# Kernel tuning notes

Hardware: AMD Instinct MI355X
Metric: run time of the kernel (lower is better)

Reference implementation:

```python
import jax, jax.numpy as jnp
import numpy as np

N = 50000      # nodes
E = 800000     # edges (avg degree 16)
IN_DIM = 128
H = 4          # attention heads
D = 32         # hidden dim per head
NEG_SLOPE = 0.2


def setup_inputs() -> dict:
    key = jax.random.key(0)
    ks = jax.random.split(key, 9)
    x = jax.random.normal(ks[0], (N, IN_DIM), dtype=jnp.float32)
    src = jax.random.randint(ks[1], (E,), 0, N, dtype=jnp.int64)
    dst = jax.random.randint(ks[2], (E,), 0, N, dtype=jnp.int64)
    # layer 0: IN_DIM -> H*D ; layer 1: H*D -> H*D
    s0 = 1.0 / np.sqrt(IN_DIM)
    s1 = 1.0 / np.sqrt(H * D)
    W1 = jax.random.normal(ks[3], (H * D, IN_DIM), dtype=jnp.float32) * s0
    al1 = jax.random.normal(ks[4], (1, H, D), dtype=jnp.float32) * s1
    ar1 = jax.random.normal(ks[5], (1, H, D), dtype=jnp.float32) * s1
    W2 = jax.random.normal(ks[6], (H * D, H * D), dtype=jnp.float32) * s1
    al2 = jax.random.normal(ks[7], (1, H, D), dtype=jnp.float32) * s1
    ar2 = jax.random.normal(ks[8], (1, H, D), dtype=jnp.float32) * s1
    return {"x": x, "src": src, "dst": dst, "W1": W1, "al1": al1, "ar1": ar1,
            "W2": W2, "al2": al2, "ar2": ar2}


def gat_conv(h, src, dst, W, al, ar):
    """DGL-style GATConv. h: [N, F_in] -> [N, H, D], with ELU activation."""
    feat = (h @ W.T).reshape(N, H, D)                 # [N,H,D]
    el = jnp.sum(feat * al, axis=-1)                  # [N,H] a_l . Wh
    er = jnp.sum(feat * ar, axis=-1)                  # [N,H] a_r . Wh
    e = jax.nn.leaky_relu(el[src] + er[dst], NEG_SLOPE)  # [E,H]
    # numerically stable edge softmax over incoming edges of each dst node
    m = jax.ops.segment_max(e, dst, num_segments=N)   # [N,H]
    ee = jnp.exp(e - m[dst])                          # [E,H]
    denom = jax.ops.segment_sum(ee, dst, num_segments=N)  # [N,H]
    alpha = ee / denom[dst]                           # [E,H]
    msg = feat[src] * alpha[..., None]                # [E,H,D]
    out = jax.ops.segment_sum(msg, dst, num_segments=N)   # [N,H,D]
    return jax.nn.elu(out)


def reference(x, src, dst, W1, al1, ar1, W2, al2, ar2):
    h = gat_conv(x, src, dst, W1, al1, ar1).reshape(N, H * D)  # flatten(1)
    h = gat_conv(h, src, dst, W2, al2, ar2)                    # [N,H,D]
    return jnp.mean(h, axis=1)                                 # [N,D]
```

## Files before the change

### kernel.cpp

```cpp
#include <hip/hip_runtime.h>
#include <cmath>
#include <type_traits>

#define HEADS 4
#define FDIM 128
#define NEG 0.2f
#define NBUCK 8

typedef __attribute__((ext_vector_type(8))) __bf16 bf16x8;
typedef __attribute__((ext_vector_type(8))) _Float16 h16x8;
typedef __attribute__((ext_vector_type(4))) float f32x4;

__global__ __launch_bounds__(256) void prep_kernel(
    const float* __restrict__ W1, const float* __restrict__ al1,
    const float* __restrict__ ar1,
    const float* __restrict__ W2, const float* __restrict__ al2,
    const float* __restrict__ ar2,
    __bf16* __restrict__ wf1, __bf16* __restrict__ wext1,
    __bf16* __restrict__ wf2, __bf16* __restrict__ wext2,
    int* __restrict__ counts, int nb)
{
    const int b = blockIdx.x, tid = threadIdx.x;
    if (b < 256) {
        const float* W = (b < 128) ? W1 : W2;
        __bf16* wf = (b < 128) ? wf1 : wf2;
        int idx = (b & 127) * 256 + tid;
        int j = idx & 7;
        int r = idx >> 3;
        int c = r & 15; r >>= 4;
        int t = r & 7;  r >>= 3;
        int kq = r & 15;
        int hl = r >> 4;
        float v = W[(t * 16 + c) * 128 + kq * 8 + j];
        __bf16 hi = (__bf16)v;
        wf[idx] = (hl == 0) ? hi : (__bf16)(v - (float)hi);
    } else if (b < 258) {
        const float* W  = (b == 256) ? W1 : W2;
        const float* al = (b == 256) ? al1 : al2;
        const float* ar = (b == 256) ? ar1 : ar2;
        __bf16* wext = (b == 256) ? wext1 : wext2;
        __shared__ float val[1024];
        #pragma unroll
        for (int ch = 0; ch < 4; ++ch) {
            int idx = ch * 256 + tid;
            int c = idx >> 7, k = idx & 127;
            int h = c & 3;
            const float* a = (c < 4) ? al : ar;
            float s = 0.f;
            for (int d = 0; d < 32; ++d)
                s += a[h * 32 + d] * W[(h * 32 + d) * 128 + k];
            val[c * 128 + k] = s;
        }
        __syncthreads();
        #pragma unroll
        for (int ch = 0; ch < 16; ++ch) {
            int idx = tid * 16 + ch;
            int j = idx & 7;
            int r = idx >> 3;
            int c = r & 15; r >>= 4;
            int kq = r & 15;
            int hl = r >> 4;
            float v = (c < 8) ? val[c * 128 + kq * 8 + j] : 0.f;
            __bf16 hi = (__bf16)v;
            wext[idx] = (hl == 0) ? hi : (__bf16)(v - (float)hi);
        }
    } else {
        int i0 = ((b - 258) * 256 + tid) * 4;
        if (i0 + 3 < nb) {
            *(int4*)&counts[i0] = make_int4(0, 0, 0, 0);
        } else {
            for (int i = i0; i < nb; ++i) counts[i] = 0;
        }
    }
}

template <typename XT>
__device__ __forceinline__ void gemm_body(
    const XT* __restrict__ X, const bf16x8* __restrict__ wf,
    const bf16x8* __restrict__ wext, _Float16* __restrict__ featH,
    float* __restrict__ el, float* __restrict__ er,
    int nnodes, int tile0, int tend, int stride, bf16x8* lw)
{
    const int tid = threadIdx.x;
    const int wave = tid >> 6, lane = tid & 63;
    const int l15 = lane & 15, quad = lane >> 4;

    int tile = tile0;
    float xr[32], xn[32];

    auto loadX = [&](int tl, float* dst) {
        int nodeA = tl * 64 + wave * 16 + l15;
        bool v = nodeA < nnodes;
        if constexpr (std::is_same<XT, float>::value) {
            const float4* xp = (const float4*)(X + (size_t)nodeA * 128);
            #pragma unroll
            for (int ks = 0; ks < 4; ++ks) {
                float4 a = v ? xp[ks * 8 + quad * 2]     : make_float4(0.f, 0.f, 0.f, 0.f);
                float4 b = v ? xp[ks * 8 + quad * 2 + 1] : make_float4(0.f, 0.f, 0.f, 0.f);
                dst[ks * 8 + 0] = a.x; dst[ks * 8 + 1] = a.y;
                dst[ks * 8 + 2] = a.z; dst[ks * 8 + 3] = a.w;
                dst[ks * 8 + 4] = b.x; dst[ks * 8 + 5] = b.y;
                dst[ks * 8 + 6] = b.z; dst[ks * 8 + 7] = b.w;
            }
        } else {
            const h16x8* xp = (const h16x8*)(X + (size_t)nodeA * 128);
            #pragma unroll
            for (int ks = 0; ks < 4; ++ks) {
                h16x8 hv;
                if (v) {
                    hv = xp[ks * 4 + quad];
                } else {
                    #pragma unroll
                    for (int j = 0; j < 8; ++j) hv[j] = (_Float16)0.f;
                }
                #pragma unroll
                for (int j = 0; j < 8; ++j) dst[ks * 8 + j] = (float)hv[j];
            }
        }
    };

    loadX(tile, xr);
    for (int i = tid; i < 2048; i += 256) lw[i] = wf[i];
    __syncthreads();

    while (true) {
        int next = tile + stride;
        if (next < tend) loadX(next, xn);

        f32x4 acc[9];
        #pragma unroll
        for (int t = 0; t < 9; ++t) acc[t] = (f32x4){0.f, 0.f, 0.f, 0.f};

        #pragma unroll
        for (int ks = 0; ks < 4; ++ks) {
            bf16x8 ahi, alo;
            #pragma unroll
            for (int j = 0; j < 8; ++j) {
                float xv = xr[ks * 8 + j];
                __bf16 h = (__bf16)xv;
                ahi[j] = h;
                alo[j] = (__bf16)(xv - (float)h);
            }
            const int kq = ks * 4 + quad;

            {
                bf16x8 bh = wext[(kq) * 16 + l15];
                bf16x8 bl = wext[(16 + kq) * 16 + l15];
                acc[8] = __builtin_amdgcn_mfma_f32_16x16x32_bf16(ahi, bh, acc[8], 0, 0, 0);
                acc[8] = __builtin_amdgcn_mfma_f32_16x16x32_bf16(alo, bh, acc[8], 0, 0, 0);
                acc[8] = __builtin_amdgcn_mfma_f32_16x16x32_bf16(ahi, bl, acc[8], 0, 0, 0);
            }
            #pragma unroll
            for (int t = 0; t < 8; ++t) {
                bf16x8 bh = lw[(kq * 8 + t) * 16 + l15];
                bf16x8 bl = wf[2048 + (kq * 8 + t) * 16 + l15];
                acc[t] = __builtin_amdgcn_mfma_f32_16x16x32_bf16(ahi, bh, acc[t], 0, 0, 0);
                acc[t] = __builtin_amdgcn_mfma_f32_16x16x32_bf16(alo, bh, acc[t], 0, 0, 0);
                acc[t] = __builtin_amdgcn_mfma_f32_16x16x32_bf16(ahi, bl, acc[t], 0, 0, 0);
            }
        }

        const int nodeC = tile * 64 + wave * 16 + quad * 4;
        #pragma unroll
        for (int r = 0; r < 4; ++r) {
            int gn = nodeC + r;
            if (gn < nnodes) {
                #pragma unroll
                for (int t = 0; t < 8; ++t)
                    featH[(size_t)gn * 128 + t * 16 + l15] = (_Float16)acc[t][r];
            }
        }
        if (l15 < 8) {
            #pragma unroll
            for (int r = 0; r < 4; ++r) {
                int gn = nodeC + r;
                if (gn < nnodes) {
                    if (l15 < 4) el[gn * HEADS + l15] = acc[8][r];
                    else         er[gn * HEADS + (l15 - 4)] = acc[8][r];
                }
            }
        }

        if (next >= tend) break;
        #pragma unroll
        for (int i = 0; i < 32; ++i) xr[i] = xn[i];
        tile = next;
    }
}

__device__ __forceinline__ void hist_body(
    const int* __restrict__ src, const int* __restrict__ dst,
    int* __restrict__ counts, int* __restrict__ rank, int nedges, int shift, int b)
{
    int i0 = (b * 256 + threadIdx.x) * 8;
    if (i0 + 7 < nedges) {
        int4 d0 = *(const int4*)&dst[i0];
        int4 d1 = *(const int4*)&dst[i0 + 4];
        int4 s0 = *(const int4*)&src[i0];
        int4 s1 = *(const int4*)&src[i0 + 4];
        int4 r0, r1;
        r0.x = atomicAdd(&counts[d0.x * NBUCK + (s0.x >> shift)], 1);
        r0.y = atomicAdd(&counts[d0.y * NBUCK + (s0.y >> shift)], 1);
        r0.z = atomicAdd(&counts[d0.z * NBUCK + (s0.z >> shift)], 1);
        r0.w = atomicAdd(&counts[d0.w * NBUCK + (s0.w >> shift)], 1);
        r1.x = atomicAdd(&counts[d1.x * NBUCK + (s1.x >> shift)], 1);
        r1.y = atomicAdd(&counts[d1.y * NBUCK + (s1.y >> shift)], 1);
        r1.z = atomicAdd(&counts[d1.z * NBUCK + (s1.z >> shift)], 1);
        r1.w = atomicAdd(&counts[d1.w * NBUCK + (s1.w >> shift)], 1);
        *(int4*)&rank[i0]     = r0;
        *(int4*)&rank[i0 + 4] = r1;
    } else {
        for (int i = i0; i < nedges; ++i)
            rank[i] = atomicAdd(&counts[dst[i] * NBUCK + (src[i] >> shift)], 1);
    }
}

__device__ __forceinline__ void scatter_body(
    const int* __restrict__ src, const int* __restrict__ dst,
    const int* __restrict__ rank, const int* __restrict__ offsets,
    int* __restrict__ csr_src, int nedges, int shift, int b)
{
    int i0 = (b * 256 + threadIdx.x) * 8;
    if (i0 + 7 < nedges) {
        int4 d0 = *(const int4*)&dst[i0];
        int4 d1 = *(const int4*)&dst[i0 + 4];
        int4 r0 = *(const int4*)&rank[i0];
        int4 r1 = *(const int4*)&rank[i0 + 4];
        int4 s0 = *(const int4*)&src[i0];
        int4 s1 = *(const int4*)&src[i0 + 4];
        csr_src[offsets[d0.x * NBUCK + (s0.x >> shift)] + r0.x] = s0.x;
        csr_src[offsets[d0.y * NBUCK + (s0.y >> shift)] + r0.y] = s0.y;
        csr_src[offsets[d0.z * NBUCK + (s0.z >> shift)] + r0.z] = s0.z;
        csr_src[offsets[d0.w * NBUCK + (s0.w >> shift)] + r0.w] = s0.w;
        csr_src[offsets[d1.x * NBUCK + (s1.x >> shift)] + r1.x] = s1.x;
        csr_src[offsets[d1.y * NBUCK + (s1.y >> shift)] + r1.y] = s1.y;
        csr_src[offsets[d1.z * NBUCK + (s1.z >> shift)] + r1.z] = s1.z;
        csr_src[offsets[d1.w * NBUCK + (s1.w >> shift)] + r1.w] = s1.w;
    } else {
        for (int i = i0; i < nedges; ++i)
            csr_src[offsets[dst[i] * NBUCK + (src[i] >> shift)] + rank[i]] = src[i];
    }
}

__global__ __launch_bounds__(256) void fused_gemm_hist(
    const float* __restrict__ X, const bf16x8* __restrict__ wf,
    const bf16x8* __restrict__ wext, _Float16* __restrict__ featH,
    float* __restrict__ el, float* __restrict__ er, int nnodes,
    int t0, int tend, int gemm_blocks,
    const int* __restrict__ src, const int* __restrict__ dst,
    int* __restrict__ counts, int* __restrict__ rank, int nedges, int shift)
{
    __shared__ bf16x8 lw[2048];
    if ((int)blockIdx.x < gemm_blocks)
        gemm_body<float>(X, wf, wext, featH, el, er, nnodes,
                         t0 + blockIdx.x, tend, gemm_blocks, lw);
    else
        hist_body(src, dst, counts, rank, nedges, shift, blockIdx.x - gemm_blocks);
}

__global__ __launch_bounds__(256) void fused_gemm_scatter(
    const float* __restrict__ X, const bf16x8* __restrict__ wf,
    const bf16x8* __restrict__ wext, _Float16* __restrict__ featH,
    float* __restrict__ el, float* __restrict__ er, int nnodes,
    int t0, int tend, int gemm_blocks,
    const int* __restrict__ src, const int* __restrict__ dst,
    const int* __restrict__ rank, const int* __restrict__ offsets,
    int* __restrict__ csr_src, int nedges, int shift)
{
    __shared__ bf16x8 lw[2048];
    if ((int)blockIdx.x < gemm_blocks)
        gemm_body<float>(X, wf, wext, featH, el, er, nnodes,
                         t0 + blockIdx.x, tend, gemm_blocks, lw);
    else
        scatter_body(src, dst, rank, offsets, csr_src, nedges, shift,
                     blockIdx.x - gemm_blocks);
}

template <typename XT>
__global__ __launch_bounds__(256) void gemm_mfma_kernel(
    const XT* __restrict__ X, const bf16x8* __restrict__ wf,
    const bf16x8* __restrict__ wext, _Float16* __restrict__ featH,
    float* __restrict__ el, float* __restrict__ er, int nnodes, int ntiles)
{
    __shared__ bf16x8 lw[2048];
    gemm_body<XT>(X, wf, wext, featH, el, er, nnodes,
                  blockIdx.x, ntiles, gridDim.x, lw);
}

__global__ __launch_bounds__(256) void scan1_kernel(
    const int* __restrict__ counts, int* __restrict__ offsets,
    int* __restrict__ bsums, int n)
{
    __shared__ int wsums[4];
    const int tid = threadIdx.x, lane = tid & 63, w = tid >> 6;
    const int i = blockIdx.x * 1024 + tid * 4;

    int4 v = make_int4(0, 0, 0, 0);
    if (i + 3 < n) v = *(const int4*)&counts[i];
    else {
        if (i < n)     v.x = counts[i];
        if (i + 1 < n) v.y = counts[i + 1];
        if (i + 2 < n) v.z = counts[i + 2];
    }
    int s0 = v.x, s1 = s0 + v.y, s2 = s1 + v.z, s3 = s2 + v.w;

    int x = s3;
    #pragma unroll
    for (int off = 1; off < 64; off <<= 1) {
        int t = __shfl_up(x, off, 64);
        if (lane >= off) x += t;
    }
    if (lane == 63) wsums[w] = x;
    __syncthreads();
    int wbase = 0;
    #pragma unroll
    for (int k = 0; k < 4; ++k) if (k < w) wbase += wsums[k];

    int tbase = wbase + x - s3;
    if (i < n)     offsets[i]     = tbase;
    if (i + 1 < n) offsets[i + 1] = tbase + s0;
    if (i + 2 < n) offsets[i + 2] = tbase + s1;
    if (i + 3 < n) offsets[i + 3] = tbase + s2;
    if (tid == 255) bsums[blockIdx.x] = wbase + x;
}

__global__ __launch_bounds__(256) void scan23_kernel(
    int* __restrict__ offsets, const int* __restrict__ bsums, int n, int nedges)
{
    __shared__ int sbase;
    const int tid = threadIdx.x, b = blockIdx.x;
    if (tid < 64) {
        int s = 0;
        for (int i = tid; i < b; i += 64) s += bsums[i];
        #pragma unroll
        for (int off = 1; off < 64; off <<= 1) s += __shfl_xor(s, off, 64);
        if (tid == 0) sbase = s;
    }
    __syncthreads();
    const int base = sbase;
    const int i = b * 1024 + tid * 4;
    #pragma unroll
    for (int k = 0; k < 4; ++k)
        if (i + k < n) offsets[i + k] += base;
    if (b == 0 && tid == 0) offsets[n] = nedges;
}

template <bool MEAN>
__global__ __launch_bounds__(256) void aggregate_kernel(
    const _Float16* __restrict__ featH, const float* __restrict__ el,
    const float* __restrict__ er, const int* __restrict__ offsets,
    const int* __restrict__ csr_src, void* __restrict__ outp, int nnodes)
{
    const int n = (blockIdx.x * 256 + threadIdx.x) >> 6;
    if (n >= nnodes) return;
    const int lane = threadIdx.x & 63;
    const int g = lane >> 4, u = lane & 15, h = u >> 2;
    const int beg = offsets[n * NBUCK], end = offsets[n * NBUCK + NBUCK];
    const float ern = er[n * HEADS + h];
    const int iters = (end - beg + 3) >> 2;

    float a[8];
    #pragma unroll
    for (int p = 0; p < 8; ++p) a[p] = 0.f;
    float sw = 0.f;

    const h16x8* __restrict__ frow = (const h16x8*)featH;

    int ja = beg + g;
    int jb = ja + 4;
    bool va = ja < end, vb = jb < end;
    int sa = va ? csr_src[ja] : 0;
    int sb = vb ? csr_src[jb] : 0;
    float qa = el[sa * HEADS + h];
    float qb = el[sb * HEADS + h];
    h16x8 fa = frow[(size_t)sa * 16 + u];
    h16x8 fb = frow[(size_t)sb * 16 + u];

    for (int it = 0; it < iters; ++it) {
        int jc = ja + 8;
        bool vc = jc < end;
        int sc = vc ? csr_src[jc] : 0;
        float qc = el[sc * HEADS + h];
        h16x8 fc = frow[(size_t)sc * 16 + u];

        float e = qa + ern;
        e = e > 0.f ? e : NEG * e;
        float w = va ? __expf(e) : 0.f;
        #pragma unroll
        for (int p = 0; p < 8; ++p) a[p] += w * (float)fa[p];
        sw += w;

        ja = jb; va = vb; sa = sb; qa = qb; fa = fb;
        jb = jc; vb = vc; sb = sc; qb = qc; fb = fc;
    }

    #pragma unroll
    for (int p = 0; p < 8; ++p) {
        a[p] += __shfl_xor(a[p], 16, 64);
        a[p] += __shfl_xor(a[p], 32, 64);
    }
    sw += __shfl_xor(sw, 16, 64);
    sw += __shfl_xor(sw, 32, 64);

    float inv = sw > 0.f ? 1.f / sw : 0.f;
    float r[8];
    #pragma unroll
    for (int p = 0; p < 8; ++p) {
        float t = a[p] * inv;
        r[p] = t > 0.f ? t : expm1f(t);
    }

    if (!MEAN) {
        if (g == 0) {
            h16x8 o;
            #pragma unroll
            for (int p = 0; p < 8; ++p) o[p] = (_Float16)r[p];
            ((h16x8*)outp)[(size_t)n * 16 + u] = o;
        }
    } else {
        #pragma unroll
        for (int p = 0; p < 8; ++p) {
            r[p] += __shfl_xor(r[p], 4, 64);
            r[p] += __shfl_xor(r[p], 8, 64);
        }
        if (g == 0 && u < 4) {
            float* out = (float*)outp;
            float4* o4 = (float4*)(out + (size_t)n * 32 + u * 8);
            o4[0] = make_float4(0.25f * r[0], 0.25f * r[1], 0.25f * r[2], 0.25f * r[3]);
            o4[1] = make_float4(0.25f * r[4], 0.25f * r[5], 0.25f * r[6], 0.25f * r[7]);
        }
    }
}

extern "C" void kernel_launch(void* const* d_in, const int* in_sizes, int n_in,
                              void* d_out, int out_size, void* d_ws, size_t ws_size,
                              hipStream_t stream)
{
    const float* x   = (const float*)d_in[0];
    const int*   src = (const int*)d_in[1];
    const int*   dst = (const int*)d_in[2];
    const float* W1  = (const float*)d_in[3];
    const float* al1 = (const float*)d_in[4];
    const float* ar1 = (const float*)d_in[5];
    const float* W2  = (const float*)d_in[6];
    const float* al2 = (const float*)d_in[7];
    const float* ar2 = (const float*)d_in[8];

    const int N = in_sizes[0] / FDIM;
    const int E = in_sizes[1];
    const int NB = N * NBUCK;

    int shift = 0;
    while (((N - 1) >> shift) > (NBUCK - 1)) ++shift;

    _Float16* h1 = (_Float16*)d_ws;
    _Float16* featH = h1 + (size_t)N * FDIM;
    float* el = (float*)(featH + (size_t)N * FDIM);
    float* er = el + (size_t)N * HEADS;
    int* counts  = (int*)(er + (size_t)N * HEADS);
    int* offsets = counts + NB;
    int* rank    = offsets + (NB + 1);
    int* csr_src = rank + E;
    int* bsums   = csr_src + E;
    uintptr_t wp = ((uintptr_t)(bsums + 512) + 63) & ~(uintptr_t)63;
    __bf16* wf1   = (__bf16*)wp;
    __bf16* wext1 = wf1 + 32768;
    __bf16* wf2   = wext1 + 4096;
    __bf16* wext2 = wf2 + 32768;

    const int ntiles = (N + 63) / 64;
    const int halfT  = (ntiles + 1) / 2;
    const int gA = halfT < 256 ? halfT : 256;
    const int gB = (ntiles - halfT) < 256 ? (ntiles - halfT) : 256;
    const int edge8_grid = ((E + 7) / 8 + 255) / 256;
    const int agg_grid  = (N + 3) / 4;
    const int nscan     = (NB + 1023) / 1024;
    const int zblocks   = ((NB + 3) / 4 + 255) / 256;
    const int g2 = ntiles < 512 ? ntiles : 512;

    prep_kernel<<<258 + zblocks, 256, 0, stream>>>(
        W1, al1, ar1, W2, al2, ar2, wf1, wext1, wf2, wext2, counts, NB);

    fused_gemm_hist<<<gA + edge8_grid, 256, 0, stream>>>(
        x, (const bf16x8*)wf1, (const bf16x8*)wext1, featH, el, er, N,
        0, halfT, gA, src, dst, counts, rank, E, shift);

    scan1_kernel<<<nscan, 256, 0, stream>>>(counts, offsets, bsums, NB);
    scan23_kernel<<<nscan, 256, 0, stream>>>(offsets, bsums, NB, E);

    fused_gemm_scatter<<<gB + edge8_grid, 256, 0, stream>>>(
        x, (const bf16x8*)wf1, (const bf16x8*)wext1, featH, el, er, N,
        halfT, ntiles, gB, src, dst, rank, offsets, csr_src, E, shift);

    aggregate_kernel<false><<<agg_grid, 256, 0, stream>>>(
        featH, el, er, offsets, csr_src, (void*)h1, N);

    gemm_mfma_kernel<_Float16><<<g2, 256, 0, stream>>>(
        h1, (const bf16x8*)wf2, (const bf16x8*)wext2, featH, el, er, N, ntiles);
    aggregate_kernel<true><<<agg_grid, 256, 0, stream>>>(
        featH, el, er, offsets, csr_src, d_out, N);
}
```

Measured before the change: 248.4 us.

## Merge scan kernels with grid barrier, use native f16 MFMA for layer 2

Result: slower. 264.7 us (+6.6%).

```diff
diff --git a/kernel.cpp b/kernel.cpp
--- a/kernel.cpp
+++ b/kernel.cpp
@@ -17,13 +17,11 @@
     const float* __restrict__ W2, const float* __restrict__ al2,
     const float* __restrict__ ar2,
     __bf16* __restrict__ wf1, __bf16* __restrict__ wext1,
-    __bf16* __restrict__ wf2, __bf16* __restrict__ wext2,
-    int* __restrict__ counts, int nb)
+    _Float16* __restrict__ wf2, _Float16* __restrict__ wext2,
+    int* __restrict__ counts, int nb, int* __restrict__ bsums)
 {
     const int b = blockIdx.x, tid = threadIdx.x;
     if (b < 256) {
-        const float* W = (b < 128) ? W1 : W2;
-        __bf16* wf = (b < 128) ? wf1 : wf2;
         int idx = (b & 127) * 256 + tid;
         int j = idx & 7;
         int r = idx >> 3;
@@ -31,14 +29,19 @@
         int t = r & 7;  r >>= 3;
         int kq = r & 15;
         int hl = r >> 4;
-        float v = W[(t * 16 + c) * 128 + kq * 8 + j];
-        __bf16 hi = (__bf16)v;
-        wf[idx] = (hl == 0) ? hi : (__bf16)(v - (float)hi);
+        if (b < 128) {
+            float v = W1[(t * 16 + c) * 128 + kq * 8 + j];
+            __bf16 hi = (__bf16)v;
+            wf1[idx] = (hl == 0) ? hi : (__bf16)(v - (float)hi);
+        } else {
+            float v = W2[(t * 16 + c) * 128 + kq * 8 + j];
+            _Float16 hi = (_Float16)v;
+            wf2[idx] = (hl == 0) ? hi : (_Float16)(v - (float)hi);
+        }
     } else if (b < 258) {
         const float* W  = (b == 256) ? W1 : W2;
         const float* al = (b == 256) ? al1 : al2;
         const float* ar = (b == 256) ? ar1 : ar2;
-        __bf16* wext = (b == 256) ? wext1 : wext2;
         __shared__ float val[1024];
         #pragma unroll
         for (int ch = 0; ch < 4; ++ch) {
@@ -61,10 +64,18 @@
             int kq = r & 15;
             int hl = r >> 4;
             float v = (c < 8) ? val[c * 128 + kq * 8 + j] : 0.f;
-            __bf16 hi = (__bf16)v;
-            wext[idx] = (hl == 0) ? hi : (__bf16)(v - (float)hi);
+            if (b == 256) {
+                __bf16 hi = (__bf16)v;
+                wext1[idx] = (hl == 0) ? hi : (__bf16)(v - (float)hi);
+            } else {
+                _Float16 hi = (_Float16)v;
+                wext2[idx] = (hl == 0) ? hi : (_Float16)(v - (float)hi);
+            }
         }
     } else {
+        if (b == 258) {
+            for (int k = tid; k < 512; k += 256) bsums[k] = 0;
+        }
         int i0 = ((b - 258) * 256 + tid) * 4;
         if (i0 + 3 < nb) {
             *(int4*)&counts[i0] = make_int4(0, 0, 0, 0);
@@ -74,9 +85,8 @@
     }
 }
 
-template <typename XT>
-__device__ __forceinline__ void gemm_body(
-    const XT* __restrict__ X, const bf16x8* __restrict__ wf,
+__device__ __forceinline__ void gemm_body_f32(
+    const float* __restrict__ X, const bf16x8* __restrict__ wf,
     const bf16x8* __restrict__ wext, _Float16* __restrict__ featH,
     float* __restrict__ el, float* __restrict__ er,
     int nnodes, int tile0, int tend, int stride, bf16x8* lw)
@@ -91,31 +101,15 @@
     auto loadX = [&](int tl, float* dst) {
         int nodeA = tl * 64 + wave * 16 + l15;
         bool v = nodeA < nnodes;
-        if constexpr (std::is_same<XT, float>::value) {
-            const float4* xp = (const float4*)(X + (size_t)nodeA * 128);
-            #pragma unroll
-            for (int ks = 0; ks < 4; ++ks) {
-                float4 a = v ? xp[ks * 8 + quad * 2]     : make_float4(0.f, 0.f, 0.f, 0.f);
-                float4 b = v ? xp[ks * 8 + quad * 2 + 1] : make_float4(0.f, 0.f, 0.f, 0.f);
-                dst[ks * 8 + 0] = a.x; dst[ks * 8 + 1] = a.y;
-                dst[ks * 8 + 2] = a.z; dst[ks * 8 + 3] = a.w;
-                dst[ks * 8 + 4] = b.x; dst[ks * 8 + 5] = b.y;
-                dst[ks * 8 + 6] = b.z; dst[ks * 8 + 7] = b.w;
-            }
-        } else {
-            const h16x8* xp = (const h16x8*)(X + (size_t)nodeA * 128);
-            #pragma unroll
-            for (int ks = 0; ks < 4; ++ks) {
-                h16x8 hv;
-                if (v) {
-                    hv = xp[ks * 4 + quad];
-                } else {
-                    #pragma unroll
-                    for (int j = 0; j < 8; ++j) hv[j] = (_Float16)0.f;
-                }
-                #pragma unroll
-                for (int j = 0; j < 8; ++j) dst[ks * 8 + j] = (float)hv[j];
-            }
+        const float4* xp = (const float4*)(X + (size_t)nodeA * 128);
+        #pragma unroll
+        for (int ks = 0; ks < 4; ++ks) {
+            float4 a = v ? xp[ks * 8 + quad * 2]     : make_float4(0.f, 0.f, 0.f, 0.f);
+            float4 b = v ? xp[ks * 8 + quad * 2 + 1] : make_float4(0.f, 0.f, 0.f, 0.f);
+            dst[ks * 8 + 0] = a.x; dst[ks * 8 + 1] = a.y;
+            dst[ks * 8 + 2] = a.z; dst[ks * 8 + 3] = a.w;
+            dst[ks * 8 + 4] = b.x; dst[ks * 8 + 5] = b.y;
+            dst[ks * 8 + 6] = b.z; dst[ks * 8 + 7] = b.w;
         }
     };
 
@@ -184,6 +178,93 @@
         if (next >= tend) break;
         #pragma unroll
         for (int i = 0; i < 32; ++i) xr[i] = xn[i];
+        tile = next;
+    }
+}
+
+__device__ __forceinline__ void gemm_body_f16(
+    const _Float16* __restrict__ X, const h16x8* __restrict__ wf,
+    const h16x8* __restrict__ wext, _Float16* __restrict__ featH,
+    float* __restrict__ el, float* __restrict__ er,
+    int nnodes, int tile0, int tend, int stride, h16x8* lw)
+{
+    const int tid = threadIdx.x;
+    const int wave = tid >> 6, lane = tid & 63;
+    const int l15 = lane & 15, quad = lane >> 4;
+
+    int tile = tile0;
+    h16x8 xr[4], xn[4];
+
+    auto loadX = [&](int tl, h16x8* dst) {
+        int nodeA = tl * 64 + wave * 16 + l15;
+        bool v = nodeA < nnodes;
+        const h16x8* xp = (const h16x8*)(X + (size_t)nodeA * 128);
+        #pragma unroll
+        for (int ks = 0; ks < 4; ++ks) {
+            if (v) {
+                dst[ks] = xp[ks * 4 + quad];
+            } else {
+                #pragma unroll
+                for (int j = 0; j < 8; ++j) dst[ks][j] = (_Float16)0.f;
+            }
+        }
+    };
+
+    loadX(tile, xr);
+    for (int i = tid; i < 2048; i += 256) lw[i] = wf[i];
+    __syncthreads();
+
+    while (true) {
+        int next = tile + stride;
+        if (next < tend) loadX(next, xn);
+
+        f32x4 acc[9];
+        #pragma unroll
+        for (int t = 0; t < 9; ++t) acc[t] = (f32x4){0.f, 0.f, 0.f, 0.f};
+
+        #pragma unroll
+        for (int ks = 0; ks < 4; ++ks) {
+            h16x8 a = xr[ks];
+            const int kq = ks * 4 + quad;
+            {
+                h16x8 bh = wext[(kq) * 16 + l15];
+                h16x8 bl = wext[(16 + kq) * 16 + l15];
+                acc[8] = __builtin_amdgcn_mfma_f32_16x16x32_f16(a, bh, acc[8], 0, 0, 0);
+                acc[8] = __builtin_amdgcn_mfma_f32_16x16x32_f16(a, bl, acc[8], 0, 0, 0);
+            }
+            #pragma unroll
+            for (int t = 0; t < 8; ++t) {
+                h16x8 bh = lw[(kq * 8 + t) * 16 + l15];
+                h16x8 bl = wf[2048 + (kq * 8 + t) * 16 + l15];
+                acc[t] = __builtin_amdgcn_mfma_f32_16x16x32_f16(a, bh, acc[t], 0, 0, 0);
+                acc[t] = __builtin_amdgcn_mfma_f32_16x16x32_f16(a, bl, acc[t], 0, 0, 0);
+            }
+        }
+
+        const int nodeC = tile * 64 + wave * 16 + quad * 4;
+        #pragma unroll
+        for (int r = 0; r < 4; ++r) {
+            int gn = nodeC + r;
+            if (gn < nnodes) {
+                #pragma unroll
+                for (int t = 0; t < 8; ++t)
+                    featH[(size_t)gn * 128 + t * 16 + l15] = (_Float16)acc[t][r];
+            }
+        }
+        if (l15 < 8) {
+            #pragma unroll
+            for (int r = 0; r < 4; ++r) {
+                int gn = nodeC + r;
+                if (gn < nnodes) {
+                    if (l15 < 4) el[gn * HEADS + l15] = acc[8][r];
+                    else         er[gn * HEADS + (l15 - 4)] = acc[8][r];
+                }
+            }
+        }
+
+        if (next >= tend) break;
+        #pragma unroll
+        for (int i = 0; i < 4; ++i) xr[i] = xn[i];
         tile = next;
     }
 }
@@ -252,8 +333,8 @@
 {
     __shared__ bf16x8 lw[2048];
     if ((int)blockIdx.x < gemm_blocks)
-        gemm_body<float>(X, wf, wext, featH, el, er, nnodes,
-                         t0 + blockIdx.x, tend, gemm_blocks, lw);
+        gemm_body_f32(X, wf, wext, featH, el, er, nnodes,
+                      t0 + blockIdx.x, tend, gemm_blocks, lw);
     else
         hist_body(src, dst, counts, rank, nedges, shift, blockIdx.x - gemm_blocks);
 }
@@ -269,31 +350,31 @@
 {
     __shared__ bf16x8 lw[2048];
     if ((int)blockIdx.x < gemm_blocks)
-        gemm_body<float>(X, wf, wext, featH, el, er, nnodes,
-                         t0 + blockIdx.x, tend, gemm_blocks, lw);
+        gemm_body_f32(X, wf, wext, featH, el, er, nnodes,
+                      t0 + blockIdx.x, tend, gemm_blocks, lw);
     else
         scatter_body(src, dst, rank, offsets, csr_src, nedges, shift,
                      blockIdx.x - gemm_blocks);
 }
 
-template <typename XT>
-__global__ __launch_bounds__(256) void gemm_mfma_kernel(
-    const XT* __restrict__ X, const bf16x8* __restrict__ wf,
-    const bf16x8* __restrict__ wext, _Float16* __restrict__ featH,
+__global__ __launch_bounds__(256) void gemm_mfma_f16_kernel(
+    const _Float16* __restrict__ X, const h16x8* __restrict__ wf,
+    const h16x8* __restrict__ wext, _Float16* __restrict__ featH,
     float* __restrict__ el, float* __restrict__ er, int nnodes, int ntiles)
 {
-    __shared__ bf16x8 lw[2048];
-    gemm_body<XT>(X, wf, wext, featH, el, er, nnodes,
+    __shared__ h16x8 lw[2048];
+    gemm_body_f16(X, wf, wext, featH, el, er, nnodes,
                   blockIdx.x, ntiles, gridDim.x, lw);
 }
 
-__global__ __launch_bounds__(256) void scan1_kernel(
+__global__ __launch_bounds__(256) void scan_kernel(
     const int* __restrict__ counts, int* __restrict__ offsets,
-    int* __restrict__ bsums, int n)
+    int* __restrict__ pval, int* __restrict__ done, int n, int nedges)
 {
     __shared__ int wsums[4];
     const int tid = threadIdx.x, lane = tid & 63, w = tid >> 6;
-    const int i = blockIdx.x * 1024 + tid * 4;
+    const int b = blockIdx.x;
+    const int i = b * 1024 + tid * 4;
 
     int4 v = make_int4(0, 0, 0, 0);
     if (i + 3 < n) v = *(const int4*)&counts[i];
@@ -315,33 +396,36 @@
     int wbase = 0;
     #pragma unroll
     for (int k = 0; k < 4; ++k) if (k < w) wbase += wsums[k];
-
-    int tbase = wbase + x - s3;
-    if (i < n)     offsets[i]     = tbase;
-    if (i + 1 < n) offsets[i + 1] = tbase + s0;
-    if (i + 2 < n) offsets[i + 2] = tbase + s1;
-    if (i + 3 < n) offsets[i + 3] = tbase + s2;
-    if (tid == 255) bsums[blockIdx.x] = wbase + x;
-}
-
-__global__ __launch_bounds__(256) void scan23_kernel(
-    int* __restrict__ offsets, const int* __restrict__ bsums, int n, int nedges)
-{
-    __shared__ int sbase;
-    const int tid = threadIdx.x, b = blockIdx.x;
-    if (tid < 64) {
-        int s = 0;
-        for (int i = tid; i < b; i += 64) s += bsums[i];
-        #pragma unroll
-        for (int off = 1; off < 64; off <<= 1) s += __shfl_xor(s, off, 64);
-        if (tid == 0) sbase = s;
+    const int total = wsums[0] + wsums[1] + wsums[2] + wsums[3];
+
+    if (tid == 0) {
+        pval[b] = total;
+        __threadfence();
+        atomicAdd(done, 1);
+        while (__hip_atomic_load(done, __ATOMIC_ACQUIRE,
+                                 __HIP_MEMORY_SCOPE_AGENT) < (int)gridDim.x)
+            __builtin_amdgcn_s_sleep(2);
     }
     __syncthreads();
-    const int base = sbase;
-    const int i = b * 1024 + tid * 4;
+
+    int basep = 0;
+    for (int j = tid; j < b; j += 256) basep += pval[j];
     #pragma unroll
-    for (int k = 0; k < 4; ++k)
-        if (i + k < n) offsets[i + k] += base;
+    for (int off = 1; off < 64; off <<= 1) basep += __shfl_xor(basep, off, 64);
+    __syncthreads();
+    if (lane == 0) wsums[w] = basep;
+    __syncthreads();
+    const int base = wsums[0] + wsums[1] + wsums[2] + wsums[3];
+
+    const int tbase = base + wbase + x - s3;
+    if (i + 3 < n) {
+        *(int4*)&offsets[i] = make_int4(tbase, tbase + s0, tbase + s1, tbase + s2);
+    } else {
+        if (i < n)     offsets[i]     = tbase;
+        if (i + 1 < n) offsets[i + 1] = tbase + s0;
+        if (i + 2 < n) offsets[i + 2] = tbase + s1;
+        if (i + 3 < n) offsets[i + 3] = tbase + s2;
+    }
     if (b == 0 && tid == 0) offsets[n] = nedges;
 }
 
@@ -385,10 +469,10 @@
 
         float e = qa + ern;
         e = e > 0.f ? e : NEG * e;
-        float w = va ? __expf(e) : 0.f;
-        #pragma unroll
-        for (int p = 0; p < 8; ++p) a[p] += w * (float)fa[p];
-        sw += w;
+        float w2 = va ? __expf(e) : 0.f;
+        #pragma unroll
+        for (int p = 0; p < 8; ++p) a[p] += w2 * (float)fa[p];
+        sw += w2;
 
         ja = jb; va = vb; sa = sb; qa = qb; fa = fb;
         jb = jc; vb = vc; sb = sc; qb = qc; fb = fc;
@@ -407,7 +491,7 @@
     #pragma unroll
     for (int p = 0; p < 8; ++p) {
         float t = a[p] * inv;
-        r[p] = t > 0.f ? t : expm1f(t);
+        r[p] = t > 0.f ? t : __expf(t) - 1.f;
     }
 
     if (!MEAN) {
@@ -463,10 +547,10 @@
     int* csr_src = rank + E;
     int* bsums   = csr_src + E;
     uintptr_t wp = ((uintptr_t)(bsums + 512) + 63) & ~(uintptr_t)63;
-    __bf16* wf1   = (__bf16*)wp;
-    __bf16* wext1 = wf1 + 32768;
-    __bf16* wf2   = wext1 + 4096;
-    __bf16* wext2 = wf2 + 32768;
+    __bf16* wf1     = (__bf16*)wp;
+    __bf16* wext1   = wf1 + 32768;
+    _Float16* wf2   = (_Float16*)(wext1 + 4096);
+    _Float16* wext2 = wf2 + 32768;
 
     const int ntiles = (N + 63) / 64;
     const int halfT  = (ntiles + 1) / 2;
@@ -479,14 +563,13 @@
     const int g2 = ntiles < 512 ? ntiles : 512;
 
     prep_kernel<<<258 + zblocks, 256, 0, stream>>>(
-        W1, al1, ar1, W2, al2, ar2, wf1, wext1, wf2, wext2, counts, NB);
+        W1, al1, ar1, W2, al2, ar2, wf1, wext1, wf2, wext2, counts, NB, bsums);
 
     fused_gemm_hist<<<gA + edge8_grid, 256, 0, stream>>>(
         x, (const bf16x8*)wf1, (const bf16x8*)wext1, featH, el, er, N,
         0, halfT, gA, src, dst, counts, rank, E, shift);
 
-    scan1_kernel<<<nscan, 256, 0, stream>>>(counts, offsets, bsums, NB);
-    scan23_kernel<<<nscan, 256, 0, stream>>>(offsets, bsums, NB, E);
+    scan_kernel<<<nscan, 256, 0, stream>>>(counts, offsets, bsums, &bsums[500], NB, E);
 
     fused_gemm_scatter<<<gB + edge8_grid, 256, 0, stream>>>(
         x, (const bf16x8*)wf1, (const bf16x8*)wext1, featH, el, er, N,
@@ -495,8 +578,8 @@
     aggregate_kernel<false><<<agg_grid, 256, 0, stream>>>(
         featH, el, er, offsets, csr_src, (void*)h1, N);
 
-    gemm_mfma_kernel<_Float16><<<g2, 256, 0, stream>>>(
-        h1, (const bf16x8*)wf2, (const bf16x8*)wext2, featH, el, er, N, ntiles);
+    gemm_mfma_f16_kernel<<<g2, 256, 0, stream>>>(
+        h1, (const h16x8*)wf2, (const h16x8*)wext2, featH, el, er, N, ntiles);
     aggregate_kernel<true><<<agg_grid, 256, 0, stream>>>(
         featH, el, er, offsets, csr_src, d_out, N);
 }
```
